# Kernel optimization log

Measured on AMD Instinct MI355X. Metric: run time of the kernel, lower is better.

Reference implementation:

```python
import jax, jax.numpy as jnp
import numpy as np

HEADS = 4

def _proj(x, w, b):
    # 1x1 conv == per-pixel linear: x [B,C,H,W], w [O,C], b [O]
    return jnp.einsum('oc,bchw->bohw', w, x) + b[None, :, None, None]

def setup_inputs() -> dict:
    key = jax.random.key(0)
    ks = jax.random.split(key, 9)
    B, C, H, W = 16, 512, 32, 32
    emb = C // HEADS
    return {
        'x': jax.random.normal(ks[0], (B, C, H, W), jnp.float32),
        'wq_w': jax.random.normal(ks[1], (C, C), jnp.float32) * 0.02,
        'wq_b': jax.random.normal(ks[2], (C,), jnp.float32) * 0.02,
        'wk_w': jax.random.normal(ks[3], (C, C), jnp.float32) * 0.02,
        'wk_b': jax.random.normal(ks[4], (C,), jnp.float32) * 0.02,
        'wv_w': jax.random.normal(ks[5], (C, C), jnp.float32) * 0.02,
        'wv_b': jax.random.normal(ks[6], (C,), jnp.float32) * 0.02,
        'rh': jax.random.normal(ks[7], (1, HEADS, emb, 1, H), jnp.float32),
        'rw': jax.random.normal(ks[8], (1, HEADS, emb, W, 1), jnp.float32),
    }

def reference(x, wq_w, wq_b, wk_w, wk_b, wv_w, wv_b, rh, rw):
    B, C, H, W = x.shape
    heads = HEADS
    emb = C // heads
    scale = C ** (-0.5)
    N = H * W
    q = _proj(x, wq_w, wq_b).reshape(B, heads, emb, N).transpose(0, 1, 3, 2) * scale  # [B,h,N,d]
    kt = _proj(x, wk_w, wk_b).reshape(B, heads, emb, N)                               # [B,h,d,N]
    v = _proj(x, wv_w, wv_b).reshape(B, heads, emb, N).transpose(0, 1, 3, 2)          # [B,h,N,d]
    qkt = jnp.matmul(q, kt)                                                           # [B,h,N,N]
    # relative-position term: (rh + rw) broadcasts to [1,h,d,W,H], flattened as in source
    rt = (rh + rw).reshape(1, heads, emb, N)
    qrt = jnp.matmul(q, rt)                                                           # [B,h,N,N]
    attn = jax.nn.softmax(qkt + qrt, axis=-1)
    y = jnp.matmul(attn, v)                                                           # [B,h,N,d]
    return y.reshape(B, C, H, W)
```

## Files before the change

kernel.cpp:

```cpp
#include <hip/hip_runtime.h>
#include <hip/hip_bf16.h>
#include <cstdint>

#define NB 16
#define NC 512
#define NPIX 1024
#define NHEADS 4
#define NEMB 128

typedef short bf16x8 __attribute__((ext_vector_type(8)));
typedef float f32x4 __attribute__((ext_vector_type(4)));
typedef float f32x16 __attribute__((ext_vector_type(16)));
typedef unsigned short u16x4 __attribute__((ext_vector_type(4)));
typedef unsigned short u16x8 __attribute__((ext_vector_type(8)));

__device__ __forceinline__ unsigned short f2bf(float f) {
  union { float f; unsigned u; } c; c.f = f;
  return (unsigned short)((c.u + 0x7FFFu + ((c.u >> 16) & 1u)) >> 16);
}

__device__ __forceinline__ unsigned cvtpk_bf16(float lo, float hi) {
  unsigned r;
  asm("v_cvt_pk_bf16_f32 %0, %1, %2" : "=v"(r) : "v"(lo), "v"(hi));
  return r;
}

__device__ __forceinline__ void gload_lds16(const void* g, void* l) {
  __builtin_amdgcn_global_load_lds(
      (const __attribute__((address_space(1))) unsigned int*)g,
      (__attribute__((address_space(3))) unsigned int*)l, 16, 0, 0);
}

__global__ void k_prep_x(const float* __restrict__ x, unsigned short* __restrict__ xt) {
  __shared__ float tile[32][33];
  int bid = blockIdx.x;
  int nt = bid & 31, ct = (bid >> 5) & 15, b = bid >> 9;
  int n0 = nt * 32, c0 = ct * 32;
  int t = threadIdx.x;
  int r = t >> 3, q = t & 7;
  float4 v = *(const float4*)(x + ((size_t)(b * NC + c0 + r)) * NPIX + n0 + q * 4);
  tile[r][q * 4 + 0] = v.x; tile[r][q * 4 + 1] = v.y;
  tile[r][q * 4 + 2] = v.z; tile[r][q * 4 + 3] = v.w;
  __syncthreads();
  int cl = q * 4;
  u16x4 o;
  o[0] = f2bf(tile[cl + 0][r]); o[1] = f2bf(tile[cl + 1][r]);
  o[2] = f2bf(tile[cl + 2][r]); o[3] = f2bf(tile[cl + 3][r]);
  *(u16x4*)(xt + ((size_t)(b * NPIX + n0 + r)) * NC + c0 + cl) = o;
}

__global__ void k_prep_w(const float* __restrict__ wq, const float* __restrict__ wk,
                         const float* __restrict__ wv, unsigned short* __restrict__ wb) {
  const float* src = blockIdx.y == 0 ? wq : (blockIdx.y == 1 ? wk : wv);
  unsigned short* dst = wb + (size_t)blockIdx.y * NC * NC;
  for (int i = blockIdx.x * 256 + threadIdx.x; i < NC * NC / 4; i += gridDim.x * 256) {
    float4 v = ((const float4*)src)[i];
    u16x4 o = { f2bf(v.x), f2bf(v.y), f2bf(v.z), f2bf(v.w) };
    ((u16x4*)dst)[i] = o;
  }
}

__global__ __launch_bounds__(256, 2) void k_qkv(
    const unsigned short* __restrict__ wb, const unsigned short* __restrict__ xt,
    const float* __restrict__ qb, const float* __restrict__ kb, const float* __restrict__ vb,
    const float* __restrict__ rh, const float* __restrict__ rw,
    unsigned short* __restrict__ Qs, unsigned short* __restrict__ Kn,
    unsigned short* __restrict__ Vm) {
  __shared__ unsigned short Alds[128 * 64];
  __shared__ unsigned short Blds[128 * 64];
  int bid = blockIdx.x;
  int nt = bid & 7, mt = (bid >> 3) & 3;
  int rest = bid >> 5;
  int p = rest % 3, b = rest / 3;
  int m0 = mt * 128, n0 = nt * 128;
  const unsigned short* A = wb + (size_t)p * NC * NC + (size_t)m0 * NC;
  const unsigned short* Bx = xt + (size_t)b * NPIX * NC + (size_t)n0 * NC;
  int t = threadIdx.x;
  int lane = t & 63, wid = t >> 6;
  int wm = (wid >> 1) * 64, wn = (wid & 1) * 64;
  f32x4 acc[4][4] = {};
  for (int k0 = 0; k0 < NC; k0 += 64) {
#pragma unroll
    for (int i = 0; i < 4; i++) {
      int idx = i * 256 + t;
      int row = idx >> 3, col = (idx & 7) * 8;
      gload_lds16(A + (size_t)row * NC + k0 + col, &Alds[idx * 8]);
    }
#pragma unroll
    for (int i = 0; i < 4; i++) {
      int idx = i * 256 + t;
      int row = idx >> 3, col = (idx & 7) * 8;
      gload_lds16(Bx + (size_t)row * NC + k0 + col, &Blds[idx * 8]);
    }
    __syncthreads();
#pragma unroll
    for (int ks = 0; ks < 2; ks++) {
      int kk = ks * 32 + ((lane >> 4) << 3);
      bf16x8 af[4], bfr[4];
#pragma unroll
      for (int f = 0; f < 4; f++)
        af[f] = *(const bf16x8*)&Alds[(wm + f * 16 + (lane & 15)) * 64 + kk];
#pragma unroll
      for (int f = 0; f < 4; f++)
        bfr[f] = *(const bf16x8*)&Blds[(wn + f * 16 + (lane & 15)) * 64 + kk];
#pragma unroll
      for (int fm = 0; fm < 4; fm++)
#pragma unroll
        for (int fn = 0; fn < 4; fn++)
          acc[fm][fn] = __builtin_amdgcn_mfma_f32_16x16x32_bf16(af[fm], bfr[fn], acc[fm][fn], 0, 0, 0);
    }
    __syncthreads();
  }
  const float scale = 0.044194173824159216f * 1.4426950408889634f;
  if (p == 2) {
    char* vbase = (char*)(Vm + (size_t)(b * NHEADS + mt) * 16 * 8192);
#pragma unroll
    for (int fm = 0; fm < 4; fm++) {
#pragma unroll
      for (int r = 0; r < 4; r++) {
        int d = wm + fm * 16 + ((lane >> 4) << 2) + r;
        float bv = vb[m0 + d];
        char* vt = vbase + (size_t)d * 128;
#pragma unroll
        for (int fn = 0; fn < 4; fn++) {
          int j = n0 + wn + fn * 16 + (lane & 15);
          int tile = j >> 6, jl = j & 63;
          *(unsigned short*)(vt + tile * 16384 + (((jl * 2)) ^ ((d & 7) << 4))) =
              f2bf(acc[fm][fn][r] + bv);
        }
      }
    }
  } else if (p == 1) {
    char* kbase = (char*)(Kn + (size_t)(b * NHEADS + mt) * 16 * 8192);
#pragma unroll
    for (int fm = 0; fm < 4; fm++) {
      int e0 = wm + fm * 16 + ((lane >> 4) << 2);
#pragma unroll
      for (int fn = 0; fn < 4; fn++) {
        int j = n0 + wn + fn * 16 + (lane & 15);
        int tile = j >> 6, jl = j & 63;
        u16x4 o;
#pragma unroll
        for (int r = 0; r < 4; r++) {
          float v = acc[fm][fn][r] + kb[m0 + e0 + r];
          v += rh[(m0 + e0 + r) * 32 + (j & 31)] + rw[(m0 + e0 + r) * 32 + (j >> 5)];
          o[r] = f2bf(v);
        }
        *(u16x4*)(kbase + tile * 16384 + jl * 256 + ((2 * e0) ^ ((jl & 7) << 4))) = o;
      }
    }
  } else {
    unsigned short* dst = Qs + ((size_t)((b * NHEADS + mt) * NPIX + n0)) * NEMB;
#pragma unroll
    for (int fm = 0; fm < 4; fm++) {
      int e0 = wm + fm * 16 + ((lane >> 4) << 2);
#pragma unroll
      for (int fn = 0; fn < 4; fn++) {
        int ncol = wn + fn * 16 + (lane & 15);
        u16x4 o;
#pragma unroll
        for (int r = 0; r < 4; r++)
          o[r] = f2bf((acc[fm][fn][r] + qb[m0 + e0 + r]) * scale);
        *(u16x4*)&dst[(size_t)ncol * NEMB + e0] = o;
      }
    }
  }
}

__global__ __launch_bounds__(256, 2) void k_attn(
    const unsigned short* __restrict__ Qs, const unsigned short* __restrict__ Kp,
    const unsigned short* __restrict__ Vp, float* __restrict__ out) {
  __shared__ __align__(16) char smem[65536];
  int bid = blockIdx.x;
  int pair = bid & 63;
  int b = pair >> 2, hd = pair & 3;
  int i0 = (bid >> 6) * 128;
  int t = threadIdx.x, w = t >> 6, lane = t & 63;
  int l31 = lane & 31, hi5 = lane >> 5;
  const unsigned short* Qb = Qs + (size_t)pair * NPIX * NEMB;
  const char* Kpb = (const char*)(Kp + (size_t)pair * 16 * 8192);
  const char* Vpb = (const char*)(Vp + (size_t)pair * 16 * 8192);

  bf16x8 qf[8];
  {
    const unsigned short* qr = Qb + (size_t)(i0 + w * 32 + l31) * NEMB + hi5 * 8;
#pragma unroll
    for (int d8 = 0; d8 < 8; d8++) qf[d8] = *(const bf16x8*)(qr + d8 * 16);
  }
  f32x16 yacc[4] = {};
  float m = -3.0e38f, l = 0.f;
  const float THR = 11.5415603f;

#pragma unroll
  for (int r = 0; r < 4; r++) {
    gload_lds16(Kpb + r * 4096 + t * 16, smem + r * 4096 + t * 16);
    gload_lds16(Vpb + r * 4096 + t * 16, smem + 32768 + r * 4096 + t * 16);
  }
  __syncthreads();

  for (int tt = 0; tt < 16; tt++) {
    int cur = tt & 1;
    if (tt < 15) {
      const char* kn = Kpb + (tt + 1) * 16384;
      const char* vn = Vpb + (tt + 1) * 16384;
      char* kd = smem + (cur ^ 1) * 16384;
      char* vd = smem + 32768 + (cur ^ 1) * 16384;
#pragma unroll
      for (int r = 0; r < 4; r++) {
        gload_lds16(kn + r * 4096 + t * 16, kd + r * 4096 + t * 16);
        gload_lds16(vn + r * 4096 + t * 16, vd + r * 4096 + t * 16);
      }
    }
    const char* Kl = smem + cur * 16384;
    const char* Vl = smem + 32768 + cur * 16384;
    f32x16 sacc[2] = {};
    {
      int swz = (l31 & 7) << 4;
#pragma unroll
      for (int d8 = 0; d8 < 8; d8++) {
        int colb = (d8 * 32 + hi5 * 16) ^ swz;
        bf16x8 k0 = *(const bf16x8*)(Kl + l31 * 256 + colb);
        bf16x8 k1 = *(const bf16x8*)(Kl + (32 + l31) * 256 + colb);
        __builtin_amdgcn_s_setprio(1);
        sacc[0] = __builtin_amdgcn_mfma_f32_32x32x16_bf16(k0, qf[d8], sacc[0], 0, 0, 0);
        sacc[1] = __builtin_amdgcn_mfma_f32_32x32x16_bf16(k1, qf[d8], sacc[1], 0, 0, 0);
        __builtin_amdgcn_s_setprio(0);
      }
    }
    float pm = sacc[0][0];
#pragma unroll
    for (int i = 1; i < 16; i++) pm = fmaxf(pm, sacc[0][i]);
#pragma unroll
    for (int i = 0; i < 16; i++) pm = fmaxf(pm, sacc[1][i]);
    pm = fmaxf(pm, __shfl_xor(pm, 32));
    if (__any(pm - m > THR)) {
      float mn = fmaxf(m, pm);
      float corr = exp2f(m - mn);
      m = mn; l *= corr;
#pragma unroll
      for (int ds = 0; ds < 4; ds++)
#pragma unroll
        for (int i = 0; i < 16; i++) yacc[ds][i] *= corr;
    }
    float rs = 0.f;
#pragma unroll
    for (int c = 0; c < 2; c++)
#pragma unroll
      for (int i = 0; i < 16; i++) {
        float pv = exp2f(sacc[c][i] - m);
        sacc[c][i] = pv;
        rs += pv;
      }
    l += rs + __shfl_xor(rs, 32);
    unsigned up[2][4][2];
#pragma unroll
    for (int c = 0; c < 2; c++)
#pragma unroll
      for (int g = 0; g < 4; g++) {
        up[c][g][0] = cvtpk_bf16(sacc[c][4 * g + 0], sacc[c][4 * g + 1]);
        up[c][g][1] = cvtpk_bf16(sacc[c][4 * g + 2], sacc[c][4 * g + 3]);
      }
    bf16x8 pf[4];
    bool lo = (hi5 == 0);
#pragma unroll
    for (int c2 = 0; c2 < 4; c2++) {
      int c = c2 >> 1, gA = (c2 & 1) * 2, gB = gA + 1;
      unsigned pA0 = __shfl_xor(up[c][gA][0], 32);
      unsigned pA1 = __shfl_xor(up[c][gA][1], 32);
      unsigned pB0 = __shfl_xor(up[c][gB][0], 32);
      unsigned pB1 = __shfl_xor(up[c][gB][1], 32);
      unsigned wd[4];
      wd[0] = lo ? up[c][gA][0] : pB0;
      wd[1] = lo ? up[c][gA][1] : pB1;
      wd[2] = lo ? pA0 : up[c][gB][0];
      wd[3] = lo ? pA1 : up[c][gB][1];
      pf[c2] = *(bf16x8*)wd;
    }
    {
      int swz = (l31 & 7) << 4;
#pragma unroll
      for (int c2 = 0; c2 < 4; c2++) {
        int colb = (c2 * 32 + hi5 * 16) ^ swz;
        __builtin_amdgcn_s_setprio(1);
#pragma unroll
        for (int ds = 0; ds < 4; ds++) {
          bf16x8 vf = *(const bf16x8*)(Vl + (ds * 32 + l31) * 128 + colb);
          yacc[ds] = __builtin_amdgcn_mfma_f32_32x32x16_bf16(vf, pf[c2], yacc[ds], 0, 0, 0);
        }
        __builtin_amdgcn_s_setprio(0);
      }
    }
    __syncthreads();
  }
  float invl = 1.0f / l;
  int q = i0 + w * 32 + l31;
  float* orow = out + ((size_t)(b * NC + hd * NEMB + (q >> 3))) * NPIX + (q & 7) * NEMB;
#pragma unroll
  for (int ds = 0; ds < 4; ds++)
#pragma unroll
    for (int rg = 0; rg < 4; rg++) {
      f32x4 v;
#pragma unroll
      for (int i = 0; i < 4; i++) v[i] = yacc[ds][rg * 4 + i] * invl;
      *(f32x4*)(orow + ds * 32 + rg * 8 + hi5 * 4) = v;
    }
}

extern "C" void kernel_launch(void* const* d_in, const int* in_sizes, int n_in,
                              void* d_out, int out_size, void* d_ws, size_t ws_size,
                              hipStream_t stream) {
  const float* x  = (const float*)d_in[0];
  const float* wq = (const float*)d_in[1];
  const float* qb = (const float*)d_in[2];
  const float* wk = (const float*)d_in[3];
  const float* kb = (const float*)d_in[4];
  const float* wv = (const float*)d_in[5];
  const float* vb = (const float*)d_in[6];
  const float* rh = (const float*)d_in[7];
  const float* rw = (const float*)d_in[8];
  float* out = (float*)d_out;
  char* ws = (char*)d_ws;
  unsigned short* xt = (unsigned short*)(ws);
  unsigned short* wb = (unsigned short*)(ws + 16777216);
  unsigned short* Q  = (unsigned short*)(ws + 18350080);
  unsigned short* K  = (unsigned short*)(ws + 35127296);
  unsigned short* V  = (unsigned short*)(ws + 51904512);
  k_prep_x<<<8192, 256, 0, stream>>>(x, xt);
  k_prep_w<<<dim3(64, 3), 256, 0, stream>>>(wq, wk, wv, wb);
  k_qkv<<<1536, 256, 0, stream>>>(wb, xt, qb, kb, vb, rh, rw, Q, K, V);
  k_attn<<<512, 256, 0, stream>>>(Q, K, V, out);
}
```

Measured before the change: 111.1 us.

## Software-pipeline QK^T of next tile with softmax and PV of current tile

Restructures the attention loop so the QK^T MFMAs for tile t+1 are issued before the softmax, exp and PV work of tile t. This is done with ping-pong score accumulators and a manually unrolled pair of loop bodies. K is now prefetched two tiles ahead and V one tile ahead, with separate buffer indexing for each. The goal is to hide the serial dependency between score computation and the VALU-heavy softmax behind MFMA work. The cost is an extra 32 live accumulator registers, which raises register pressure under a 2-blocks-per-SM launch bound.

```diff
diff --git a/kernel.cpp b/kernel.cpp
--- a/kernel.cpp
+++ b/kernel.cpp
@@ -180,6 +180,7 @@
   const unsigned short* Qb = Qs + (size_t)pair * NPIX * NEMB;
   const char* Kpb = (const char*)(Kp + (size_t)pair * 16 * 8192);
   const char* Vpb = (const char*)(Vp + (size_t)pair * 16 * 8192);
+  const int swz = (l31 & 7) << 4;
 
   bf16x8 qf[8];
   {
@@ -191,47 +192,54 @@
   float m = -3.0e38f, l = 0.f;
   const float THR = 11.5415603f;
 
+  auto qkt = [&](f32x16 (&SN)[2], const char* Kl) {
+    SN[0] = (f32x16)(0.0f);
+    SN[1] = (f32x16)(0.0f);
+#pragma unroll
+    for (int d8 = 0; d8 < 8; d8++) {
+      int colb = (d8 * 32 + hi5 * 16) ^ swz;
+      bf16x8 k0 = *(const bf16x8*)(Kl + l31 * 256 + colb);
+      bf16x8 k1 = *(const bf16x8*)(Kl + (32 + l31) * 256 + colb);
+      __builtin_amdgcn_s_setprio(1);
+      SN[0] = __builtin_amdgcn_mfma_f32_32x32x16_bf16(k0, qf[d8], SN[0], 0, 0, 0);
+      SN[1] = __builtin_amdgcn_mfma_f32_32x32x16_bf16(k1, qf[d8], SN[1], 0, 0, 0);
+      __builtin_amdgcn_s_setprio(0);
+    }
+  };
+
 #pragma unroll
   for (int r = 0; r < 4; r++) {
     gload_lds16(Kpb + r * 4096 + t * 16, smem + r * 4096 + t * 16);
+    gload_lds16(Kpb + 16384 + r * 4096 + t * 16, smem + 16384 + r * 4096 + t * 16);
     gload_lds16(Vpb + r * 4096 + t * 16, smem + 32768 + r * 4096 + t * 16);
   }
   __syncthreads();
 
-  for (int tt = 0; tt < 16; tt++) {
-    int cur = tt & 1;
-    if (tt < 15) {
-      const char* kn = Kpb + (tt + 1) * 16384;
+  f32x16 sA[2], sB[2];
+  qkt(sA, smem);
+  __syncthreads();
+
+  auto body = [&](f32x16 (&SC)[2], f32x16 (&SN)[2], int tt, bool last) {
+    if (tt <= 13) {
+      const char* kn = Kpb + (tt + 2) * 16384;
+      char* kd = smem + (tt & 1) * 16384;
+#pragma unroll
+      for (int r = 0; r < 4; r++)
+        gload_lds16(kn + r * 4096 + t * 16, kd + r * 4096 + t * 16);
+    }
+    if (tt <= 14) {
       const char* vn = Vpb + (tt + 1) * 16384;
-      char* kd = smem + (cur ^ 1) * 16384;
-      char* vd = smem + 32768 + (cur ^ 1) * 16384;
-#pragma unroll
-      for (int r = 0; r < 4; r++) {
-        gload_lds16(kn + r * 4096 + t * 16, kd + r * 4096 + t * 16);
+      char* vd = smem + 32768 + ((tt + 1) & 1) * 16384;
+#pragma unroll
+      for (int r = 0; r < 4; r++)
         gload_lds16(vn + r * 4096 + t * 16, vd + r * 4096 + t * 16);
-      }
-    }
-    const char* Kl = smem + cur * 16384;
-    const char* Vl = smem + 32768 + cur * 16384;
-    f32x16 sacc[2] = {};
-    {
-      int swz = (l31 & 7) << 4;
-#pragma unroll
-      for (int d8 = 0; d8 < 8; d8++) {
-        int colb = (d8 * 32 + hi5 * 16) ^ swz;
-        bf16x8 k0 = *(const bf16x8*)(Kl + l31 * 256 + colb);
-        bf16x8 k1 = *(const bf16x8*)(Kl + (32 + l31) * 256 + colb);
-        __builtin_amdgcn_s_setprio(1);
-        sacc[0] = __builtin_amdgcn_mfma_f32_32x32x16_bf16(k0, qf[d8], sacc[0], 0, 0, 0);
-        sacc[1] = __builtin_amdgcn_mfma_f32_32x32x16_bf16(k1, qf[d8], sacc[1], 0, 0, 0);
-        __builtin_amdgcn_s_setprio(0);
-      }
-    }
-    float pm = sacc[0][0];
-#pragma unroll
-    for (int i = 1; i < 16; i++) pm = fmaxf(pm, sacc[0][i]);
-#pragma unroll
-    for (int i = 0; i < 16; i++) pm = fmaxf(pm, sacc[1][i]);
+    }
+    if (tt <= 14) qkt(SN, smem + ((tt + 1) & 1) * 16384);
+    float pm = SC[0][0];
+#pragma unroll
+    for (int i = 1; i < 16; i++) pm = fmaxf(pm, SC[0][i]);
+#pragma unroll
+    for (int i = 0; i < 16; i++) pm = fmaxf(pm, SC[1][i]);
     pm = fmaxf(pm, __shfl_xor(pm, 32));
     if (__any(pm - m > THR)) {
       float mn = fmaxf(m, pm);
@@ -247,8 +255,8 @@
     for (int c = 0; c < 2; c++)
 #pragma unroll
       for (int i = 0; i < 16; i++) {
-        float pv = exp2f(sacc[c][i] - m);
-        sacc[c][i] = pv;
+        float pv = exp2f(SC[c][i] - m);
+        SC[c][i] = pv;
         rs += pv;
       }
     l += rs + __shfl_xor(rs, 32);
@@ -257,8 +265,8 @@
     for (int c = 0; c < 2; c++)
 #pragma unroll
       for (int g = 0; g < 4; g++) {
-        up[c][g][0] = cvtpk_bf16(sacc[c][4 * g + 0], sacc[c][4 * g + 1]);
-        up[c][g][1] = cvtpk_bf16(sacc[c][4 * g + 2], sacc[c][4 * g + 3]);
+        up[c][g][0] = cvtpk_bf16(SC[c][4 * g + 0], SC[c][4 * g + 1]);
+        up[c][g][1] = cvtpk_bf16(SC[c][4 * g + 2], SC[c][4 * g + 3]);
       }
     bf16x8 pf[4];
     bool lo = (hi5 == 0);
@@ -277,7 +285,7 @@
       pf[c2] = *(bf16x8*)wd;
     }
     {
-      int swz = (l31 & 7) << 4;
+      const char* Vl = smem + 32768 + (tt & 1) * 16384;
 #pragma unroll
       for (int c2 = 0; c2 < 4; c2++) {
         int colb = (c2 * 32 + hi5 * 16) ^ swz;
@@ -290,8 +298,14 @@
         __builtin_amdgcn_s_setprio(0);
       }
     }
-    __syncthreads();
-  }
+    if (!last) __syncthreads();
+  };
+
+  for (int ti = 0; ti < 8; ti++) {
+    body(sA, sB, 2 * ti, false);
+    body(sB, sA, 2 * ti + 1, ti == 7);
+  }
+
   float invl = 1.0f / l;
   int q = i0 + w * 32 + l31;
   float* orow = out + ((size_t)(b * NC + hd * NEMB + (q >> 3))) * NPIX + (q & 7) * NEMB;
```

Result: no change. 110.4 us (-0.7%).
